# Performance work log

Hardware: AMD Instinct MI355X
Metric: run time of the kernel (lower is better)

The kernel has to match this reference:

```python
import jax, jax.numpy as jnp
import numpy as np

N_NODES = 50000
N_EDGES = 800000
F_DIM = 128
K_RBF = 5
NUM_BLOCKS = 5
NUM_RES = 2  # residuals ModuleList is overwritten; only num_atom_residual layers exist
NUM_ELEM = 20
CUTOFF = 10.0
LOG2 = float(np.log(2.0))


def shifted_softplus(x):
    return jax.nn.softplus(x) - LOG2


def rbf_expand(D):
    # D: [E]; ExponentialRBF with cutoff=10, K=5.
    # softplus(softplus_inverse(x)) == x, so centers/widths are the raw values.
    centers = jnp.linspace(1.0, float(np.exp(-CUTOFF)), K_RBF)          # [K]
    width = jnp.float32((0.5 / ((1.0 - np.exp(-CUTOFF)) / K_RBF)) ** 2)  # scalar
    x = D / CUTOFF
    x3 = x ** 3; x4 = x3 * x; x5 = x4 * x
    cut = jnp.where(x < 1.0, 1.0 - 6.0 * x5 + 15.0 * x4 - 10.0 * x3, 0.0)  # [E]
    return cut[:, None] * jnp.exp(-width * (jnp.exp(-D)[:, None] - centers) ** 2)  # [E,K]


def residual(x, w1, b1, w2, b2):
    # ResidualLayer: x + dense2(dense1(act(x))) (dropout = identity in eval)
    y = shifted_softplus(x)
    return x + (y @ w1.T + b1) @ w2.T + b2


def setup_inputs() -> dict:
    key = jax.random.key(0)
    ks = jax.random.split(key, 20)
    s = 1.0 / np.sqrt(F_DIM)
    B, R = NUM_BLOCKS, NUM_RES
    inp = {
        'atom_types': jax.random.randint(ks[0], (N_NODES,), 0, NUM_ELEM),
        'edge_src': jax.random.randint(ks[1], (N_EDGES,), 0, N_NODES),
        'edge_dst': jax.random.randint(ks[2], (N_EDGES,), 0, N_NODES),
        'pos': jax.random.normal(ks[3], (N_NODES, 3), jnp.float32) * 3.0,
        'emb_table': jax.random.normal(ks[4], (NUM_ELEM, F_DIM), jnp.float32),
        'k2f_w': jax.random.normal(ks[5], (B, F_DIM, K_RBF), jnp.float32) * 0.4,
        'wi': jax.random.normal(ks[6], (B, F_DIM, F_DIM), jnp.float32) * s,
        'bi': jnp.zeros((B, F_DIM), jnp.float32),
        'wj': jax.random.normal(ks[7], (B, F_DIM, F_DIM), jnp.float32) * s,
        'bj': jnp.zeros((B, F_DIM), jnp.float32),
        'wd': jax.random.normal(ks[8], (B, F_DIM, F_DIM), jnp.float32) * s,
        'bd': jnp.zeros((B, F_DIM), jnp.float32),
        'u': jax.random.uniform(ks[9], (B, F_DIM), jnp.float32),
        'res_w1': jax.random.normal(ks[10], (B, R, F_DIM, F_DIM), jnp.float32) * s,
        'res_b1': jnp.zeros((B, R, F_DIM), jnp.float32),
        'res_w2': jax.random.normal(ks[11], (B, R, F_DIM, F_DIM), jnp.float32) * s,
        'res_b2': jnp.zeros((B, R, F_DIM), jnp.float32),
    }
    return inp


def reference(atom_types, edge_src, edge_dst, pos, emb_table,
              k2f_w, wi, bi, wj, bj, wd, bd, u,
              res_w1, res_b1, res_w2, res_b2):
    # edge distances and RBF features are geometry-only: compute once
    dist = jnp.linalg.norm(pos[edge_src] - pos[edge_dst], axis=-1)  # [E]
    rbf = rbf_expand(dist)                                          # [E,K]

    h = emb_table[atom_types]                                       # [N,F]
    for b in range(NUM_BLOCKS):
        x = shifted_softplus(h)  # pre-activation (dropout = identity)
        # dense_i / dense_j are linear -> apply on nodes, then gather per edge
        hi = x @ wi[b].T + bi[b]
        hj = x @ wj[b].T + bj[b]
        ai = hi[edge_dst]                                           # [E,F] target i
        g = rbf @ k2f_w[b].T                                        # [E,F]
        aj = g * hj[edge_src]                                       # [E,F]
        m = ai + aj
        for r in range(NUM_RES):
            m = residual(m, res_w1[b, r], res_b1[b, r], res_w2[b, r], res_b2[b, r])
        m = shifted_softplus(m)
        new = u[b] * ai + m @ wd[b].T + bd[b]
        for r in range(NUM_RES):  # same residual layers reused (as in source)
            new = residual(new, res_w1[b, r], res_b1[b, r], res_w2[b, r], res_b2[b, r])
        h = jax.ops.segment_sum(new, edge_dst, num_segments=N_NODES)  # aggr='add'
    return h
```

## Files before the change

kernel.cpp:

```cpp
#include <hip/hip_runtime.h>
#include <stdint.h>

#define FD 128
#define NNODES 50000
#define NEDGES 800000
#define EB 64
#define NWG (NEDGES / EB)

typedef __attribute__((ext_vector_type(8))) short v8s;
typedef __attribute__((ext_vector_type(4))) float v4f;

__device__ __forceinline__ unsigned short f2bf(float f) {
  union { float f; unsigned int u; } v; v.f = f;
  unsigned int r = v.u + 0x7fffu + ((v.u >> 16) & 1u);
  return (unsigned short)(r >> 16);
}
__device__ __forceinline__ float bf2f(unsigned short b) {
  union { unsigned int u; float f; } v; v.u = ((unsigned int)b) << 16;
  return v.f;
}
__device__ __forceinline__ float sspf(float x) {
  float e = __expf(-fabsf(x));
  return fmaxf(x, 0.0f) + __logf(1.0f + e) - 0.6931471805599453f;
}
__device__ __forceinline__ uint2 pack4(float a, float b, float c, float d) {
  uint2 r;
  r.x = (unsigned)f2bf(a) | ((unsigned)f2bf(b) << 16);
  r.y = (unsigned)f2bf(c) | ((unsigned)f2bf(d) << 16);
  return r;
}

__device__ __forceinline__ void load_bfrag(const unsigned short* __restrict__ wfrag,
                                           int l, v8s (&Wf)[2][4]) {
#pragma unroll
  for (int ni = 0; ni < 2; ni++)
#pragma unroll
    for (int kk = 0; kk < 4; kk++)
      Wf[ni][kk] = *(const v8s*)(wfrag + (((ni << 2) + kk) << 9) + (l << 3));
}


__global__ void hist_kernel(const int* __restrict__ ed, int* __restrict__ hist) {
  int e = blockIdx.x * 256 + threadIdx.x;
  if (e < NEDGES) atomicAdd(&hist[ed[e]], 1);
}

__global__ void scan_kernel(const int* __restrict__ hist, int* __restrict__ cursor) {
  __shared__ int buf[1024];
  __shared__ int carry_s;
  int tid = threadIdx.x;
  if (tid == 0) carry_s = 0;
  __syncthreads();
  for (int base = 0; base < NNODES; base += 1024) {
    int i = base + tid;
    int v = (i < NNODES) ? hist[i] : 0;
    buf[tid] = v;
    __syncthreads();
    for (int off = 1; off < 1024; off <<= 1) {
      int t = (tid >= off) ? buf[tid - off] : 0;
      __syncthreads();
      buf[tid] += t;
      __syncthreads();
    }
    int incl = buf[tid];
    int c = carry_s;
    if (i < NNODES) cursor[i] = c + incl - v;
    __syncthreads();
    if (tid == 1023) carry_s = c + incl;
    __syncthreads();
  }
}

__global__ void scatter_kernel(const int* __restrict__ es, const int* __restrict__ ed,
                               int* __restrict__ cursor, int* __restrict__ es_s,
                               int* __restrict__ ed_s) {
  int e = blockIdx.x * 256 + threadIdx.x;
  if (e >= NEDGES) return;
  int d = ed[e];
  int p = atomicAdd(&cursor[d], 1);
  es_s[p] = es[e];
  ed_s[p] = d;
}


__global__ void rbf_kernel(const int* __restrict__ es, const int* __restrict__ ed,
                           const float* __restrict__ pos, float* __restrict__ rbf) {
  int e = blockIdx.x * 256 + threadIdx.x;
  if (e >= NEDGES) return;
  int s = es[e], d = ed[e];
  float dx = pos[s * 3 + 0] - pos[d * 3 + 0];
  float dy = pos[s * 3 + 1] - pos[d * 3 + 1];
  float dz = pos[s * 3 + 2] - pos[d * 3 + 2];
  float D = sqrtf(dx * dx + dy * dy + dz * dz);
  float x = D * 0.1f;
  float cut = 0.0f;
  if (x < 1.0f) {
    float x3 = x * x * x, x4 = x3 * x, x5 = x4 * x;
    cut = 1.0f - 6.0f * x5 + 15.0f * x4 - 10.0f * x3;
  }
  float eD = __expf(-D);
  float em10 = __expf(-10.0f);
  float wdt = 2.5f / (1.0f - em10);
  wdt = wdt * wdt;
#pragma unroll
  for (int k = 0; k < 5; k++) {
    float ck = 1.0f + (float)k * 0.25f * (em10 - 1.0f);
    float t = eD - ck;
    rbf[e * 5 + k] = cut * __expf(-wdt * t * t);
  }
}

__global__ void wconv_kernel(const float* __restrict__ wi, const float* __restrict__ wj,
                             const float* __restrict__ wd, const float* __restrict__ w1,
                             const float* __restrict__ w2, unsigned short* __restrict__ wimg2) {
  int i = blockIdx.x * 256 + threadIdx.x;
  if (i >= 5 * 7 * 16384) return;
  int b = i / (7 * 16384);
  int r = i - b * 7 * 16384;
  int mtx = r >> 14;
  int off = r & 16383;
  int j = off & 7;
  int l = (off >> 3) & 63;
  int kk = (off >> 9) & 3;
  int nt = off >> 11;
  int row = nt * 16 + (l & 15);
  int col = kk * 32 + (l >> 4) * 8 + j;
  const float* src;
  switch (mtx) {
    case 0: src = wi + (size_t)b * 16384; break;
    case 1: src = wj + (size_t)b * 16384; break;
    case 2: src = wd + (size_t)b * 16384; break;
    case 3: src = w1 + (size_t)(b * 2 + 0) * 16384; break;
    case 4: src = w2 + (size_t)(b * 2 + 0) * 16384; break;
    case 5: src = w1 + (size_t)(b * 2 + 1) * 16384; break;
    default: src = w2 + (size_t)(b * 2 + 1) * 16384; break;
  }
  wimg2[(size_t)(b * 7 + mtx) * 16384 + off] = f2bf(src[row * 128 + col]);
}

__global__ void h0_kernel(const int* __restrict__ at, const float* __restrict__ emb,
                          float* __restrict__ h) {
  int i = blockIdx.x * 256 + threadIdx.x;
  int n = i >> 7, c = i & 127;
  h[i] = emb[at[n] * FD + c];
}


__global__ __launch_bounds__(256, 4) void node_kernel(
    const float* __restrict__ h, const unsigned short* __restrict__ wblk,
    const float* __restrict__ bi, const float* __restrict__ bj,
    float* __restrict__ hi_f, unsigned short* __restrict__ hj_bf)
{
  __shared__ __align__(16) unsigned short ACT[FD * FD];
  const int tid = threadIdx.x;
  const int wv = tid >> 6;
  const int l = tid & 63;
  const int lc = l & 15;
  const int lg = l >> 4;
  const int cq = wv * 32 + lg * 4;
  const int n0 = blockIdx.x * 128;

  {
    int row = tid >> 1;
    int ch = (tid & 1) * 64;
    int n = n0 + row;
    int x8 = (row & 7) << 3;
#pragma unroll
    for (int q = 0; q < 16; q++) {
      int ce = ch + q * 4;
      v4f hv = (v4f){0.f, 0.f, 0.f, 0.f};
      if (n < NNODES) hv = *(const v4f*)&h[(size_t)n * FD + ce];
      uint2 p = pack4(sspf(hv[0]), sspf(hv[1]), sspf(hv[2]), sspf(hv[3]));
      *(uint2*)&ACT[row * FD + (ce ^ x8)] = p;
    }
  }

  v8s Wfi[2][4], Wfj[2][4];
  load_bfrag(wblk + 0 * 16384 + wv * 4096, l, Wfi);
  load_bfrag(wblk + 1 * 16384 + wv * 4096, l, Wfj);
  v4f biq[2], bjq[2];
#pragma unroll
  for (int ni = 0; ni < 2; ni++) {
    biq[ni] = *(const v4f*)&bi[cq + ni * 16];
    bjq[ni] = *(const v4f*)&bj[cq + ni * 16];
  }
  __syncthreads();

  const int x8 = (lc & 7) << 3;
#pragma unroll 1
  for (int ti = 0; ti < 8; ti++) {
    int node = ti * 16 + lc;
    v8s Af[4];
#pragma unroll
    for (int kk = 0; kk < 4; kk++)
      Af[kk] = *(const v8s*)&ACT[node * FD + ((kk * 32 + lg * 8) ^ x8)];
    v4f ai[2], aj[2];
#pragma unroll
    for (int ni = 0; ni < 2; ni++) { ai[ni] = biq[ni]; aj[ni] = bjq[ni]; }
#pragma unroll
    for (int ni = 0; ni < 2; ni++)
#pragma unroll
      for (int kk = 0; kk < 4; kk++) {
        ai[ni] = __builtin_amdgcn_mfma_f32_16x16x32_bf16(Wfi[ni][kk], Af[kk], ai[ni], 0, 0, 0);
        aj[ni] = __builtin_amdgcn_mfma_f32_16x16x32_bf16(Wfj[ni][kk], Af[kk], aj[ni], 0, 0, 0);
      }
    int n = n0 + node;
    if (n < NNODES) {
#pragma unroll
      for (int ni = 0; ni < 2; ni++) {
        *(v4f*)&hi_f[(size_t)n * FD + cq + ni * 16] = ai[ni];
        *(uint2*)&hj_bf[(size_t)n * FD + cq + ni * 16] =
            pack4(aj[ni][0], aj[ni][1], aj[ni][2], aj[ni][3]);
      }
    }
  }
}


__global__ __launch_bounds__(256, 4) void edge_kernel(
    const float* __restrict__ hi_f, const unsigned short* __restrict__ hj_bf,
    const float* __restrict__ rbf, const int* __restrict__ esrc,
    const int* __restrict__ edst, const unsigned short* __restrict__ wblk,
    const float* __restrict__ rb1, const float* __restrict__ rb2,
    const float* __restrict__ bd, const float* __restrict__ uvec,
    const float* __restrict__ k2f, float* __restrict__ outp)
{
  __shared__ __align__(16) unsigned short ACTb[2][EB * FD];
  __shared__ float BIAS[6 * FD];
  __shared__ float RBF5[EB * 5];
  __shared__ int EDG[2 * EB];
  __shared__ int SEGID[EB];
  __shared__ int SEGD[EB];
  __shared__ int nseg_s, share_lo_s, share_hi_s;

  const int tid = threadIdx.x;
  const int wv = tid >> 6;
  const int l = tid & 63;
  const int lc = l & 15;
  const int lg = l >> 4;
  const int cq = wv * 32 + lg * 4;
  const int x8 = (lc & 7) << 3;

  int wg;
  {
    const int q = NWG >> 3, r = NWG & 7;
    int x = blockIdx.x & 7, idx = blockIdx.x >> 3;
    wg = (x < r ? x * (q + 1) : r * (q + 1) + (x - r) * q) + idx;
  }
  const int e0 = wg * EB;

  for (int i = tid; i < 2 * EB; i += 256)
    EDG[i] = (i < EB) ? esrc[e0 + i] : edst[e0 + i - EB];
  for (int i = tid; i < EB * 5; i += 256) RBF5[i] = rbf[e0 * 5 + i];
  for (int i = tid; i < 6 * FD; i += 256) {
    int which = i >> 7, c = i & 127;
    float v;
    switch (which) {
      case 0: v = rb1[c]; break;
      case 1: v = rb2[c]; break;
      case 2: v = rb1[FD + c]; break;
      case 3: v = rb2[FD + c]; break;
      case 4: v = bd[c]; break;
      default: v = uvec[c]; break;
    }
    BIAS[i] = v;
  }

  v4f kcq[2][5];
#pragma unroll
  for (int ni = 0; ni < 2; ni++)
#pragma unroll
    for (int w = 0; w < 5; w++)
      kcq[ni][w] = *(const v4f*)&k2f[(cq + ni * 16) * 5 + w * 4];

  __syncthreads();

  if (tid < 64) {
    int d = EDG[EB + tid];
    int pd = (tid == 0) ? -1 : EDG[EB + tid - 1];
    bool bnd = (tid == 0) || (d != pd);
    unsigned long long msk = __ballot(bnd);
    int sid = (int)__popcll(msk & ((2ull << tid) - 1)) - 1;
    SEGID[tid] = sid;
    if (bnd) SEGD[sid] = d;
    if (tid == 0) {
      nseg_s = (int)__popcll(msk);
      share_lo_s = (e0 > 0) && (d == edst[e0 - 1]);
    }
    if (tid == 63) share_hi_s = (e0 + EB < NEDGES) && (d == edst[e0 + EB]);
  }

  int dN[4];
  v4f m[2][4];
#pragma unroll
  for (int ei = 0; ei < 4; ei++) {
    int row = ei * 16 + lc;
    int s = EDG[row];
    int d = EDG[EB + row];
    dN[ei] = d;
    float r5[5];
#pragma unroll
    for (int k = 0; k < 5; k++) r5[k] = RBF5[row * 5 + k];
#pragma unroll
    for (int ni = 0; ni < 2; ni++) {
      int c = cq + ni * 16;
      v4f ai = *(const v4f*)&hi_f[(size_t)d * FD + c];
      uint2 hp = *(const uint2*)&hj_bf[(size_t)s * FD + c];
      float hjf[4] = {bf2f((unsigned short)(hp.x & 0xffff)), bf2f((unsigned short)(hp.x >> 16)),
                      bf2f((unsigned short)(hp.y & 0xffff)), bf2f((unsigned short)(hp.y >> 16))};
#pragma unroll
      for (int r = 0; r < 4; r++) {
        float g = 0.f;
#pragma unroll
        for (int k = 0; k < 5; k++) {
          int fi = r * 5 + k;
          g += r5[k] * kcq[ni][fi >> 2][fi & 3];
        }
        m[ni][ei][r] = ai[r] + g * hjf[r];
      }
      *(uint2*)&ACTb[0][row * FD + (c ^ x8)] =
          pack4(sspf(m[ni][ei][0]), sspf(m[ni][ei][1]), sspf(m[ni][ei][2]), sspf(m[ni][ei][3]));
    }
  }

  int buf = 0;
#pragma unroll 1
  for (int L = 0; L < 9; L++) {
    int mat = (L == 4) ? 2 : ((L < 4) ? 3 + L : L - 2);
    v8s Wf[2][4];
    load_bfrag(wblk + mat * 16384 + wv * 4096, l, Wf);

    v4f acc[2][4];
    if (L == 4) {
      v4f uq[2], bq[2];
#pragma unroll
      for (int ni = 0; ni < 2; ni++) {
        uq[ni] = *(const v4f*)&BIAS[5 * FD + cq + ni * 16];
        bq[ni] = *(const v4f*)&BIAS[4 * FD + cq + ni * 16];
      }
#pragma unroll
      for (int ei = 0; ei < 4; ei++) {
        int d = dN[ei];
#pragma unroll
        for (int ni = 0; ni < 2; ni++) {
          v4f ai = *(const v4f*)&hi_f[(size_t)d * FD + cq + ni * 16];
#pragma unroll
          for (int r = 0; r < 4; r++) acc[ni][ei][r] = uq[ni][r] * ai[r] + bq[ni][r];
        }
      }
    } else {
      int bidx = (L < 4) ? L : L - 5;
      v4f bq[2];
#pragma unroll
      for (int ni = 0; ni < 2; ni++) bq[ni] = *(const v4f*)&BIAS[bidx * FD + cq + ni * 16];
#pragma unroll
      for (int ei = 0; ei < 4; ei++)
#pragma unroll
        for (int ni = 0; ni < 2; ni++) acc[ni][ei] = bq[ni];
    }

    __syncthreads();

    const unsigned short* A = &ACTb[buf][0];
#pragma unroll
    for (int ei = 0; ei < 4; ei++) {
      int rb = (ei * 16 + lc) * FD;
      v8s Af[4];
#pragma unroll
      for (int kk = 0; kk < 4; kk++)
        Af[kk] = *(const v8s*)&A[rb + ((kk * 32 + lg * 8) ^ x8)];
#pragma unroll
      for (int ni = 0; ni < 2; ni++)
#pragma unroll
        for (int kk = 0; kk < 4; kk++)
          acc[ni][ei] = __builtin_amdgcn_mfma_f32_16x16x32_bf16(Wf[ni][kk], Af[kk],
                                                               acc[ni][ei], 0, 0, 0);
    }

    const bool isAcc = (L == 1) || (L == 3) || (L == 6) || (L == 8);
    if (L == 4) {
#pragma unroll
      for (int ei = 0; ei < 4; ei++)
#pragma unroll
        for (int ni = 0; ni < 2; ni++) m[ni][ei] = acc[ni][ei];
    } else if (isAcc) {
#pragma unroll
      for (int ei = 0; ei < 4; ei++)
#pragma unroll
        for (int ni = 0; ni < 2; ni++) m[ni][ei] += acc[ni][ei];
    }

    if (L < 8) {
      const bool wssp = isAcc || (L == 4);
      unsigned short* An = &ACTb[buf ^ 1][0];
#pragma unroll
      for (int ei = 0; ei < 4; ei++) {
        int rb = (ei * 16 + lc) * FD;
#pragma unroll
        for (int ni = 0; ni < 2; ni++) {
          uint2 p;
          if (wssp)
            p = pack4(sspf(m[ni][ei][0]), sspf(m[ni][ei][1]),
                      sspf(m[ni][ei][2]), sspf(m[ni][ei][3]));
          else
            p = pack4(acc[ni][ei][0], acc[ni][ei][1], acc[ni][ei][2], acc[ni][ei][3]);
          *(uint2*)&An[rb + ((cq + ni * 16) ^ x8)] = p;
        }
      }
    }
    buf ^= 1;
  }

  __syncthreads();
  float* SEGF = (float*)&ACTb[0][0];
  const int ns = nseg_s;
  for (int i = tid; i < ns * FD; i += 256) SEGF[i] = 0.f;
  __syncthreads();

  {
    int sid[4];
#pragma unroll
    for (int ei = 0; ei < 4; ei++) sid[ei] = SEGID[ei * 16 + lc];
#pragma unroll
    for (int ni = 0; ni < 2; ni++) {
      v4f run = m[ni][0];
      int cs = sid[0];
#pragma unroll
      for (int ei = 1; ei < 4; ei++) {
        if (sid[ei] == cs) {
          run += m[ni][ei];
        } else {
#pragma unroll
          for (int r = 0; r < 4; r++)
            atomicAdd(&SEGF[cs * FD + cq + ni * 16 + r], run[r]);
          run = m[ni][ei];
          cs = sid[ei];
        }
      }
#pragma unroll
      for (int r = 0; r < 4; r++)
        atomicAdd(&SEGF[cs * FD + cq + ni * 16 + r], run[r]);
    }
  }
  __syncthreads();

  {
    const int shlo = share_lo_s, shhi = share_hi_s;
    for (int i = tid; i < ns * 32; i += 256) {
      int s = i >> 5;
      int c4 = (i & 31) * 4;
      int d = SEGD[s];
      v4f v = *(v4f*)&SEGF[s * FD + c4];
      bool boundary = (s == 0 && shlo) || (s == ns - 1 && shhi);
      float* dst = &outp[(size_t)d * FD + c4];
      if (boundary) {
#pragma unroll
        for (int r = 0; r < 4; r++) atomicAdd(dst + r, v[r]);
      } else {
        *(v4f*)dst = v;
      }
    }
  }
}

extern "C" void kernel_launch(void* const* d_in, const int* in_sizes, int n_in,
                              void* d_out, int out_size, void* d_ws, size_t ws_size,
                              hipStream_t stream) {
  (void)in_sizes; (void)n_in; (void)out_size; (void)ws_size;
  const int* at = (const int*)d_in[0];
  const int* es = (const int*)d_in[1];
  const int* ed = (const int*)d_in[2];
  const float* pos = (const float*)d_in[3];
  const float* emb = (const float*)d_in[4];
  const float* k2f = (const float*)d_in[5];
  const float* wi = (const float*)d_in[6];
  const float* bi = (const float*)d_in[7];
  const float* wj = (const float*)d_in[8];
  const float* bj = (const float*)d_in[9];
  const float* wd = (const float*)d_in[10];
  const float* bd = (const float*)d_in[11];
  const float* u = (const float*)d_in[12];
  const float* rw1 = (const float*)d_in[13];
  const float* rb1 = (const float*)d_in[14];
  const float* rw2 = (const float*)d_in[15];
  const float* rb2 = (const float*)d_in[16];

  char* w = (char*)d_ws;
  float* rbf = (float*)w;                     w += (size_t)NEDGES * 5 * 4;
  float* hi_f = (float*)w;                    w += (size_t)NNODES * FD * 4;
  unsigned short* hj_bf = (unsigned short*)w; w += (size_t)NNODES * FD * 2;
  float* hA = (float*)w;                      w += (size_t)NNODES * FD * 4;
  unsigned short* wimg2 = (unsigned short*)w; w += (size_t)5 * 7 * 16384 * 2;
  int* hist = (int*)w;                        w += (size_t)NNODES * 4;
  int* cursor = (int*)w;                      w += (size_t)NNODES * 4;
  int* es_s = (int*)w;                        w += (size_t)NEDGES * 4;
  int* ed_s = (int*)w;                        w += (size_t)NEDGES * 4;

  hipMemsetAsync(hist, 0, (size_t)NNODES * 4, stream);
  hist_kernel<<<(NEDGES + 255) / 256, 256, 0, stream>>>(ed, hist);
  scan_kernel<<<1, 1024, 0, stream>>>(hist, cursor);
  scatter_kernel<<<(NEDGES + 255) / 256, 256, 0, stream>>>(es, ed, cursor, es_s, ed_s);

  rbf_kernel<<<(NEDGES + 255) / 256, 256, 0, stream>>>(es_s, ed_s, pos, rbf);
  wconv_kernel<<<(5 * 7 * 16384 + 255) / 256, 256, 0, stream>>>(wi, wj, wd, rw1, rw2, wimg2);
  h0_kernel<<<(NNODES * FD) / 256, 256, 0, stream>>>(at, emb, hA);

  float* hcur = hA;
  for (int b = 0; b < 5; b++) {
    node_kernel<<<(NNODES + 127) / 128, 256, 0, stream>>>(
        hcur, wimg2 + (size_t)b * 7 * 16384, bi + b * FD, bj + b * FD, hi_f, hj_bf);
    float* tgt = (b & 1) ? hA : (float*)d_out;
    hipMemsetAsync(tgt, 0, (size_t)NNODES * FD * 4, stream);
    edge_kernel<<<NWG, 256, 0, stream>>>(
        hi_f, hj_bf, rbf, es_s, ed_s, wimg2 + (size_t)b * 7 * 16384,
        rb1 + (size_t)b * 2 * FD, rb2 + (size_t)b * 2 * FD, bd + b * FD,
        u + b * FD, k2f + (size_t)b * FD * 5, tgt);
    hcur = tgt;
  }
}
```

Baseline: 6.035 ms.

## Make each wave own 16 edges end to end, streaming weights from global

Restructures the edge kernel so each wave handles its own 16 edges across all output columns, using a private LDS activation tile. This removes the per-layer block-wide barriers and the double-buffered shared activation array. Weight fragments are now loaded straight from global inside the MFMA loop instead of being held in registers, and the RBF filter is computed from a transposed k2f table in LDS. The segment reduction is processed in chunks of 32 segments to fit the smaller LDS, and launch bounds drop to 3 blocks per SM. The cost is 4x more weight traffic per block and more barriers in the reduction stage.

```diff
diff --git a/kernel.cpp b/kernel.cpp
--- a/kernel.cpp
+++ b/kernel.cpp
@@ -28,15 +28,6 @@
   r.x = (unsigned)f2bf(a) | ((unsigned)f2bf(b) << 16);
   r.y = (unsigned)f2bf(c) | ((unsigned)f2bf(d) << 16);
   return r;
-}
-
-__device__ __forceinline__ void load_bfrag(const unsigned short* __restrict__ wfrag,
-                                           int l, v8s (&Wf)[2][4]) {
-#pragma unroll
-  for (int ni = 0; ni < 2; ni++)
-#pragma unroll
-    for (int kk = 0; kk < 4; kk++)
-      Wf[ni][kk] = *(const v8s*)(wfrag + (((ni << 2) + kk) << 9) + (l << 3));
 }
 
 
@@ -176,8 +167,13 @@
   }
 
   v8s Wfi[2][4], Wfj[2][4];
-  load_bfrag(wblk + 0 * 16384 + wv * 4096, l, Wfi);
-  load_bfrag(wblk + 1 * 16384 + wv * 4096, l, Wfj);
+#pragma unroll
+  for (int ni = 0; ni < 2; ni++)
+#pragma unroll
+    for (int kk = 0; kk < 4; kk++) {
+      Wfi[ni][kk] = *(const v8s*)(wblk + 0 * 16384 + (wv * 2 + ni) * 2048 + kk * 512 + l * 8);
+      Wfj[ni][kk] = *(const v8s*)(wblk + 1 * 16384 + (wv * 2 + ni) * 2048 + kk * 512 + l * 8);
+    }
   v4f biq[2], bjq[2];
 #pragma unroll
   for (int ni = 0; ni < 2; ni++) {
@@ -217,7 +213,7 @@
 }
 
 
-__global__ __launch_bounds__(256, 4) void edge_kernel(
+__global__ __launch_bounds__(256, 3) void edge_kernel(
     const float* __restrict__ hi_f, const unsigned short* __restrict__ hj_bf,
     const float* __restrict__ rbf, const int* __restrict__ esrc,
     const int* __restrict__ edst, const unsigned short* __restrict__ wblk,
@@ -225,8 +221,9 @@
     const float* __restrict__ bd, const float* __restrict__ uvec,
     const float* __restrict__ k2f, float* __restrict__ outp)
 {
-  __shared__ __align__(16) unsigned short ACTb[2][EB * FD];
+  __shared__ __align__(16) unsigned short ACT[4][16 * FD];
   __shared__ float BIAS[6 * FD];
+  __shared__ float K2T[5 * FD];
   __shared__ float RBF5[EB * 5];
   __shared__ int EDG[2 * EB];
   __shared__ int SEGID[EB];
@@ -238,8 +235,6 @@
   const int l = tid & 63;
   const int lc = l & 15;
   const int lg = l >> 4;
-  const int cq = wv * 32 + lg * 4;
-  const int x8 = (lc & 7) << 3;
 
   int wg;
   {
@@ -265,14 +260,10 @@
     }
     BIAS[i] = v;
   }
-
-  v4f kcq[2][5];
-#pragma unroll
-  for (int ni = 0; ni < 2; ni++)
-#pragma unroll
-    for (int w = 0; w < 5; w++)
-      kcq[ni][w] = *(const v4f*)&k2f[(cq + ni * 16) * 5 + w * 4];
-
+  for (int i = tid; i < 5 * FD; i += 256) {
+    int k = i >> 7, f = i & 127;
+    K2T[i] = k2f[f * 5 + k];
+  }
   __syncthreads();
 
   if (tid < 64) {
@@ -290,168 +281,133 @@
     if (tid == 63) share_hi_s = (e0 + EB < NEDGES) && (d == edst[e0 + EB]);
   }
 
-  int dN[4];
-  v4f m[2][4];
-#pragma unroll
-  for (int ei = 0; ei < 4; ei++) {
-    int row = ei * 16 + lc;
-    int s = EDG[row];
-    int d = EDG[EB + row];
-    dN[ei] = d;
-    float r5[5];
-#pragma unroll
-    for (int k = 0; k < 5; k++) r5[k] = RBF5[row * 5 + k];
-#pragma unroll
-    for (int ni = 0; ni < 2; ni++) {
-      int c = cq + ni * 16;
-      v4f ai = *(const v4f*)&hi_f[(size_t)d * FD + c];
-      uint2 hp = *(const uint2*)&hj_bf[(size_t)s * FD + c];
-      float hjf[4] = {bf2f((unsigned short)(hp.x & 0xffff)), bf2f((unsigned short)(hp.x >> 16)),
-                      bf2f((unsigned short)(hp.y & 0xffff)), bf2f((unsigned short)(hp.y >> 16))};
-#pragma unroll
-      for (int r = 0; r < 4; r++) {
-        float g = 0.f;
-#pragma unroll
-        for (int k = 0; k < 5; k++) {
-          int fi = r * 5 + k;
-          g += r5[k] * kcq[ni][fi >> 2][fi & 3];
-        }
-        m[ni][ei][r] = ai[r] + g * hjf[r];
-      }
-      *(uint2*)&ACTb[0][row * FD + (c ^ x8)] =
-          pack4(sspf(m[ni][ei][0]), sspf(m[ni][ei][1]), sspf(m[ni][ei][2]), sspf(m[ni][ei][3]));
-    }
-  }
-
-  int buf = 0;
+  const int myE = wv * 16 + lc;
+  const int nsrc = EDG[myE];
+  const int ndst = EDG[EB + myE];
+  unsigned short* AW = &ACT[wv][0];
+  const int xsw = (lc & 7) << 2;
+  const int rowe = lc * FD;
+
+  float r5[5];
+#pragma unroll
+  for (int k = 0; k < 5; k++) r5[k] = RBF5[myE * 5 + k];
+
+  v4f g[8];
+#pragma unroll
+  for (int t = 0; t < 8; t++) g[t] = (v4f){0.f, 0.f, 0.f, 0.f};
+#pragma unroll
+  for (int k = 0; k < 5; k++) {
+    float rk = r5[k];
+#pragma unroll
+    for (int t = 0; t < 8; t++) {
+      v4f kc = *(const v4f*)&K2T[k * FD + (t * 4 + lg) * 4];
+#pragma unroll
+      for (int r = 0; r < 4; r++) g[t][r] += rk * kc[r];
+    }
+  }
+
+  v4f m[8];
+#pragma unroll
+  for (int t = 0; t < 8; t++) {
+    int fq = (t * 4 + lg) * 4;
+    v4f ai = *(const v4f*)&hi_f[(size_t)ndst * FD + fq];
+    uint2 hp = *(const uint2*)&hj_bf[(size_t)nsrc * FD + fq];
+    float hjf[4] = {bf2f((unsigned short)(hp.x & 0xffff)), bf2f((unsigned short)(hp.x >> 16)),
+                    bf2f((unsigned short)(hp.y & 0xffff)), bf2f((unsigned short)(hp.y >> 16))};
+#pragma unroll
+    for (int r = 0; r < 4; r++) m[t][r] = ai[r] + g[t][r] * hjf[r];
+    *(uint2*)&AW[rowe + (((t * 4 + lg) ^ xsw) << 2)] =
+        pack4(sspf(m[t][0]), sspf(m[t][1]), sspf(m[t][2]), sspf(m[t][3]));
+  }
+
 #pragma unroll 1
   for (int L = 0; L < 9; L++) {
     int mat = (L == 4) ? 2 : ((L < 4) ? 3 + L : L - 2);
-    v8s Wf[2][4];
-    load_bfrag(wblk + mat * 16384 + wv * 4096, l, Wf);
-
-    v4f acc[2][4];
+    const unsigned short* wfb = wblk + mat * 16384 + l * 8;
+
+    v4f acc[8];
     if (L == 4) {
-      v4f uq[2], bq[2];
-#pragma unroll
-      for (int ni = 0; ni < 2; ni++) {
-        uq[ni] = *(const v4f*)&BIAS[5 * FD + cq + ni * 16];
-        bq[ni] = *(const v4f*)&BIAS[4 * FD + cq + ni * 16];
-      }
-#pragma unroll
-      for (int ei = 0; ei < 4; ei++) {
-        int d = dN[ei];
-#pragma unroll
-        for (int ni = 0; ni < 2; ni++) {
-          v4f ai = *(const v4f*)&hi_f[(size_t)d * FD + cq + ni * 16];
-#pragma unroll
-          for (int r = 0; r < 4; r++) acc[ni][ei][r] = uq[ni][r] * ai[r] + bq[ni][r];
-        }
+#pragma unroll
+      for (int t = 0; t < 8; t++) {
+        int fq = (t * 4 + lg) * 4;
+        v4f uq = *(const v4f*)&BIAS[5 * FD + fq];
+        v4f bq = *(const v4f*)&BIAS[4 * FD + fq];
+        v4f ai = *(const v4f*)&hi_f[(size_t)ndst * FD + fq];
+#pragma unroll
+        for (int r = 0; r < 4; r++) acc[t][r] = uq[r] * ai[r] + bq[r];
       }
     } else {
       int bidx = (L < 4) ? L : L - 5;
-      v4f bq[2];
-#pragma unroll
-      for (int ni = 0; ni < 2; ni++) bq[ni] = *(const v4f*)&BIAS[bidx * FD + cq + ni * 16];
-#pragma unroll
-      for (int ei = 0; ei < 4; ei++)
-#pragma unroll
-        for (int ni = 0; ni < 2; ni++) acc[ni][ei] = bq[ni];
-    }
-
-    __syncthreads();
-
-    const unsigned short* A = &ACTb[buf][0];
-#pragma unroll
-    for (int ei = 0; ei < 4; ei++) {
-      int rb = (ei * 16 + lc) * FD;
-      v8s Af[4];
+#pragma unroll
+      for (int t = 0; t < 8; t++)
+        acc[t] = *(const v4f*)&BIAS[bidx * FD + (t * 4 + lg) * 4];
+    }
+
+    v8s Af[4];
+#pragma unroll
+    for (int kk = 0; kk < 4; kk++)
+      Af[kk] = *(const v8s*)&AW[rowe + (((8 * kk + 2 * lg) ^ xsw) << 2)];
+
+#pragma unroll
+    for (int t = 0; t < 8; t++) {
 #pragma unroll
       for (int kk = 0; kk < 4; kk++)
-        Af[kk] = *(const v8s*)&A[rb + ((kk * 32 + lg * 8) ^ x8)];
-#pragma unroll
-      for (int ni = 0; ni < 2; ni++)
-#pragma unroll
-        for (int kk = 0; kk < 4; kk++)
-          acc[ni][ei] = __builtin_amdgcn_mfma_f32_16x16x32_bf16(Wf[ni][kk], Af[kk],
-                                                               acc[ni][ei], 0, 0, 0);
+        acc[t] = __builtin_amdgcn_mfma_f32_16x16x32_bf16(
+            *(const v8s*)(wfb + t * 2048 + kk * 512), Af[kk], acc[t], 0, 0, 0);
     }
 
     const bool isAcc = (L == 1) || (L == 3) || (L == 6) || (L == 8);
     if (L == 4) {
 #pragma unroll
-      for (int ei = 0; ei < 4; ei++)
-#pragma unroll
-        for (int ni = 0; ni < 2; ni++) m[ni][ei] = acc[ni][ei];
+      for (int t = 0; t < 8; t++) m[t] = acc[t];
     } else if (isAcc) {
 #pragma unroll
-      for (int ei = 0; ei < 4; ei++)
-#pragma unroll
-        for (int ni = 0; ni < 2; ni++) m[ni][ei] += acc[ni][ei];
+      for (int t = 0; t < 8; t++) m[t] += acc[t];
     }
 
     if (L < 8) {
       const bool wssp = isAcc || (L == 4);
-      unsigned short* An = &ACTb[buf ^ 1][0];
-#pragma unroll
-      for (int ei = 0; ei < 4; ei++) {
-        int rb = (ei * 16 + lc) * FD;
-#pragma unroll
-        for (int ni = 0; ni < 2; ni++) {
-          uint2 p;
-          if (wssp)
-            p = pack4(sspf(m[ni][ei][0]), sspf(m[ni][ei][1]),
-                      sspf(m[ni][ei][2]), sspf(m[ni][ei][3]));
-          else
-            p = pack4(acc[ni][ei][0], acc[ni][ei][1], acc[ni][ei][2], acc[ni][ei][3]);
-          *(uint2*)&An[rb + ((cq + ni * 16) ^ x8)] = p;
-        }
-      }
-    }
-    buf ^= 1;
+#pragma unroll
+      for (int t = 0; t < 8; t++) {
+        uint2 p;
+        if (wssp)
+          p = pack4(sspf(m[t][0]), sspf(m[t][1]), sspf(m[t][2]), sspf(m[t][3]));
+        else
+          p = pack4(acc[t][0], acc[t][1], acc[t][2], acc[t][3]);
+        *(uint2*)&AW[rowe + (((t * 4 + lg) ^ xsw) << 2)] = p;
+      }
+    }
   }
 
   __syncthreads();
-  float* SEGF = (float*)&ACTb[0][0];
+  float* SEGF = (float*)&ACT[0][0];
   const int ns = nseg_s;
-  for (int i = tid; i < ns * FD; i += 256) SEGF[i] = 0.f;
-  __syncthreads();
-
-  {
-    int sid[4];
-#pragma unroll
-    for (int ei = 0; ei < 4; ei++) sid[ei] = SEGID[ei * 16 + lc];
-#pragma unroll
-    for (int ni = 0; ni < 2; ni++) {
-      v4f run = m[ni][0];
-      int cs = sid[0];
-#pragma unroll
-      for (int ei = 1; ei < 4; ei++) {
-        if (sid[ei] == cs) {
-          run += m[ni][ei];
-        } else {
-#pragma unroll
-          for (int r = 0; r < 4; r++)
-            atomicAdd(&SEGF[cs * FD + cq + ni * 16 + r], run[r]);
-          run = m[ni][ei];
-          cs = sid[ei];
-        }
-      }
-#pragma unroll
-      for (int r = 0; r < 4; r++)
-        atomicAdd(&SEGF[cs * FD + cq + ni * 16 + r], run[r]);
-    }
-  }
-  __syncthreads();
-
-  {
-    const int shlo = share_lo_s, shhi = share_hi_s;
-    for (int i = tid; i < ns * 32; i += 256) {
+  const int mySeg = SEGID[myE];
+  const int shlo = share_lo_s, shhi = share_hi_s;
+
+#pragma unroll 1
+  for (int base = 0; base < ns; base += 32) {
+    int cnt = min(32, ns - base);
+    for (int i = tid; i < cnt * FD; i += 256) SEGF[i] = 0.f;
+    __syncthreads();
+    if (mySeg >= base && mySeg < base + 32) {
+      int sb = (mySeg - base) * FD;
+#pragma unroll
+      for (int t = 0; t < 8; t++) {
+        int fq = (t * 4 + lg) * 4;
+#pragma unroll
+        for (int r = 0; r < 4; r++)
+          atomicAdd(&SEGF[sb + fq + r], m[t][r]);
+      }
+    }
+    __syncthreads();
+    for (int i = tid; i < cnt * 32; i += 256) {
       int s = i >> 5;
       int c4 = (i & 31) * 4;
-      int d = SEGD[s];
+      int gs = base + s;
+      int d = SEGD[gs];
       v4f v = *(v4f*)&SEGF[s * FD + c4];
-      bool boundary = (s == 0 && shlo) || (s == ns - 1 && shhi);
+      bool boundary = (gs == 0 && shlo) || (gs == ns - 1 && shhi);
       float* dst = &outp[(size_t)d * FD + c4];
       if (boundary) {
 #pragma unroll
@@ -460,6 +416,7 @@
         *(v4f*)dst = v;
       }
     }
+    __syncthreads();
   }
 }
 
```

Result: slower. 6.933 ms (+14.9%).

## Single-buffer edge activations to cut LDS and raise occupancy to six waves

Applied to the files above, without the earlier changes.

The edge kernel's double-buffered activation tile in LDS becomes a single buffer, with an extra barrier between the MFMA reads and the writes of the next activation. The segment-sum reduction is split into chunks of 32 segments so it fits in the smaller buffer, and launch bounds rise from 4 to 6 blocks per CU. The bf16 pair packing now uses a byte-permute instruction. The aim is higher occupancy to hide gather latency, paid for with an extra barrier per layer, chunked reduction loops and tighter register limits that may cause spills.

```diff
diff --git a/kernel.cpp b/kernel.cpp
--- a/kernel.cpp
+++ b/kernel.cpp
@@ -23,11 +23,14 @@
   float e = __expf(-fabsf(x));
   return fmaxf(x, 0.0f) + __logf(1.0f + e) - 0.6931471805599453f;
 }
+__device__ __forceinline__ unsigned bfpair(float a, float b) {
+  union { float f; unsigned u; } x, y; x.f = a; y.f = b;
+  unsigned ra = x.u + 0x7fffu + ((x.u >> 16) & 1u);
+  unsigned rb = y.u + 0x7fffu + ((y.u >> 16) & 1u);
+  return __builtin_amdgcn_perm(rb, ra, 0x07060302);
+}
 __device__ __forceinline__ uint2 pack4(float a, float b, float c, float d) {
-  uint2 r;
-  r.x = (unsigned)f2bf(a) | ((unsigned)f2bf(b) << 16);
-  r.y = (unsigned)f2bf(c) | ((unsigned)f2bf(d) << 16);
-  return r;
+  uint2 r; r.x = bfpair(a, b); r.y = bfpair(c, d); return r;
 }
 
 __device__ __forceinline__ void load_bfrag(const unsigned short* __restrict__ wfrag,
@@ -217,7 +220,7 @@
 }
 
 
-__global__ __launch_bounds__(256, 4) void edge_kernel(
+__global__ __launch_bounds__(256, 6) void edge_kernel(
     const float* __restrict__ hi_f, const unsigned short* __restrict__ hj_bf,
     const float* __restrict__ rbf, const int* __restrict__ esrc,
     const int* __restrict__ edst, const unsigned short* __restrict__ wblk,
@@ -225,7 +228,7 @@
     const float* __restrict__ bd, const float* __restrict__ uvec,
     const float* __restrict__ k2f, float* __restrict__ outp)
 {
-  __shared__ __align__(16) unsigned short ACTb[2][EB * FD];
+  __shared__ __align__(16) unsigned short ACT[EB * FD];
   __shared__ float BIAS[6 * FD];
   __shared__ float RBF5[EB * 5];
   __shared__ int EDG[2 * EB];
@@ -318,12 +321,11 @@
         }
         m[ni][ei][r] = ai[r] + g * hjf[r];
       }
-      *(uint2*)&ACTb[0][row * FD + (c ^ x8)] =
+      *(uint2*)&ACT[row * FD + (c ^ x8)] =
           pack4(sspf(m[ni][ei][0]), sspf(m[ni][ei][1]), sspf(m[ni][ei][2]), sspf(m[ni][ei][3]));
     }
   }
 
-  int buf = 0;
 #pragma unroll 1
   for (int L = 0; L < 9; L++) {
     int mat = (L == 4) ? 2 : ((L < 4) ? 3 + L : L - 2);
@@ -361,7 +363,7 @@
 
     __syncthreads();
 
-    const unsigned short* A = &ACTb[buf][0];
+    const unsigned short* A = &ACT[0];
 #pragma unroll
     for (int ei = 0; ei < 4; ei++) {
       int rb = (ei * 16 + lc) * FD;
@@ -390,9 +392,10 @@
         for (int ni = 0; ni < 2; ni++) m[ni][ei] += acc[ni][ei];
     }
 
+    __syncthreads();
+
     if (L < 8) {
       const bool wssp = isAcc || (L == 4);
-      unsigned short* An = &ACTb[buf ^ 1][0];
 #pragma unroll
       for (int ei = 0; ei < 4; ei++) {
         int rb = (ei * 16 + lc) * FD;
@@ -404,23 +407,25 @@
                       sspf(m[ni][ei][2]), sspf(m[ni][ei][3]));
           else
             p = pack4(acc[ni][ei][0], acc[ni][ei][1], acc[ni][ei][2], acc[ni][ei][3]);
-          *(uint2*)&An[rb + ((cq + ni * 16) ^ x8)] = p;
+          *(uint2*)&ACT[rb + ((cq + ni * 16) ^ x8)] = p;
         }
       }
     }
-    buf ^= 1;
-  }
-
-  __syncthreads();
-  float* SEGF = (float*)&ACTb[0][0];
+  }
+
+  float* SEGF = (float*)&ACT[0];
   const int ns = nseg_s;
-  for (int i = tid; i < ns * FD; i += 256) SEGF[i] = 0.f;
-  __syncthreads();
-
-  {
-    int sid[4];
-#pragma unroll
-    for (int ei = 0; ei < 4; ei++) sid[ei] = SEGID[ei * 16 + lc];
+  const int shlo = share_lo_s, shhi = share_hi_s;
+  int sid[4];
+#pragma unroll
+  for (int ei = 0; ei < 4; ei++) sid[ei] = SEGID[ei * 16 + lc];
+
+#pragma unroll 1
+  for (int base = 0; base < ns; base += 32) {
+    int cnt = min(32, ns - base);
+    for (int i = tid; i < cnt * FD; i += 256) SEGF[i] = 0.f;
+    __syncthreads();
+
 #pragma unroll
     for (int ni = 0; ni < 2; ni++) {
       v4f run = m[ni][0];
@@ -430,28 +435,30 @@
         if (sid[ei] == cs) {
           run += m[ni][ei];
         } else {
-#pragma unroll
-          for (int r = 0; r < 4; r++)
-            atomicAdd(&SEGF[cs * FD + cq + ni * 16 + r], run[r]);
+          if (cs >= base && cs < base + 32) {
+#pragma unroll
+            for (int r = 0; r < 4; r++)
+              atomicAdd(&SEGF[(cs - base) * FD + cq + ni * 16 + r], run[r]);
+          }
           run = m[ni][ei];
           cs = sid[ei];
         }
       }
-#pragma unroll
-      for (int r = 0; r < 4; r++)
-        atomicAdd(&SEGF[cs * FD + cq + ni * 16 + r], run[r]);
-    }
-  }
-  __syncthreads();
-
-  {
-    const int shlo = share_lo_s, shhi = share_hi_s;
-    for (int i = tid; i < ns * 32; i += 256) {
+      if (cs >= base && cs < base + 32) {
+#pragma unroll
+        for (int r = 0; r < 4; r++)
+          atomicAdd(&SEGF[(cs - base) * FD + cq + ni * 16 + r], run[r]);
+      }
+    }
+    __syncthreads();
+
+    for (int i = tid; i < cnt * 32; i += 256) {
       int s = i >> 5;
       int c4 = (i & 31) * 4;
-      int d = SEGD[s];
+      int gs = base + s;
+      int d = SEGD[gs];
       v4f v = *(v4f*)&SEGF[s * FD + c4];
-      bool boundary = (s == 0 && shlo) || (s == ns - 1 && shhi);
+      bool boundary = (gs == 0 && shlo) || (gs == ns - 1 && shhi);
       float* dst = &outp[(size_t)d * FD + c4];
       if (boundary) {
 #pragma unroll
@@ -460,6 +467,7 @@
         *(v4f*)dst = v;
       }
     }
+    __syncthreads();
   }
 }
 
```

Measured after the change: 8.992 ms. 49.0% more time.
